# Performance work log

Measured on AMD Instinct MI355X. Metric: run time of the kernel, lower is better.

Reference implementation:

```python
import jax, jax.numpy as jnp
import numpy as np

NORM_EPS = 1e-6
QUANT_EPS = 1e-8


def setup_inputs() -> dict:
    key = jax.random.key(0)
    k1, k2 = jax.random.split(key)
    B, S, D_IN, D_OUT = 2, 4096, 2048, 2048
    x = jax.random.normal(k1, (B, S, D_IN), dtype=jnp.float32)
    # master fp32 weights (kaiming-uniform-ish scale)
    weight = jax.random.uniform(k2, (D_OUT, D_IN), dtype=jnp.float32,
                                minval=-1.0, maxval=1.0) * (1.0 / np.sqrt(D_IN))
    norm_weight = jnp.ones((D_IN,), dtype=jnp.float32)
    return {"x": x, "weight": weight, "norm_weight": norm_weight}


def _rmsnorm(x, gain):
    rms = jnp.sqrt(jnp.mean(x * x, axis=-1, keepdims=True) + NORM_EPS)
    return x / rms * gain


def _ternary_quantize(w):
    gamma = jnp.mean(jnp.abs(w))                       # absmean scale (scalar)
    w_q = jnp.clip(jnp.round(w / (gamma + QUANT_EPS)), -1.0, 1.0)
    return w_q, gamma


def reference(x, weight, norm_weight):
    # 1) RMSNorm input
    xn = _rmsnorm(x, norm_weight)
    # 2) ternary-quantize weights {-1,0,+1} with absmean gamma
    w_q, gamma = _ternary_quantize(weight)
    # 3) matmul with ternary weights, 4) scale by gamma
    # xn: [B,S,Din], w_q: [Dout,Din] -> [B,S,Dout]
    return jnp.einsum('bsd,od->bso', xn, w_q) * gamma
```

## Files before the change

### kernel.cpp

```cpp
#include <hip/hip_runtime.h>
#include <hip/hip_bf16.h>
#include <stdint.h>

typedef unsigned short u16;
typedef signed char i8;

#define D_INNER 2048
#define D_OUTER 2048
#define MROWS   8192
#define W_ELEMS (D_OUTER * D_INNER)
#define NPART   1024

#define BM 256
#define BN 256
#define BK 128
#define NKT (D_INNER / BK)
#define LDS_TOTAL 65536

typedef __attribute__((ext_vector_type(4))) float f32x4;
typedef __attribute__((ext_vector_type(4))) int   i32x4;
typedef __attribute__((ext_vector_type(16))) int  i32x16;

__global__ __launch_bounds__(256) void prep_kernel(const float* __restrict__ x,
                            const float* __restrict__ g,
                            const float* __restrict__ w,
                            i8* __restrict__ xn, float* __restrict__ srow,
                            float* __restrict__ partials) {
  __shared__ float red[4];
  __shared__ float redm[4];
  int t = threadIdx.x;
  int lane = t & 63, wvi = t >> 6;

  if (blockIdx.x >= MROWS) {
    int p = blockIdx.x - MROWS;
    int base = p * 1024;
    float s = 0.f;
#pragma unroll
    for (int r = 0; r < 4; ++r) {
      f32x4 v = ((const f32x4*)w)[base + r * 256 + t];
      s += fabsf(v[0]) + fabsf(v[1]) + fabsf(v[2]) + fabsf(v[3]);
    }
    for (int off = 32; off; off >>= 1) s += __shfl_down(s, off, 64);
    if (lane == 0) red[wvi] = s;
    __syncthreads();
    if (t == 0) partials[p] = red[0] + red[1] + red[2] + red[3];
    return;
  }

  int row = blockIdx.x;
  const f32x4* xr = (const f32x4*)(x + (size_t)row * D_INNER);
  i8* xo = xn + (size_t)row * D_INNER;

  f32x4 v0 = __builtin_nontemporal_load(&xr[t]);
  f32x4 v1 = __builtin_nontemporal_load(&xr[t + 256]);
  const f32x4* gr = (const f32x4*)g;
  f32x4 g0 = gr[t], g1 = gr[t + 256];

  float s = v0[0]*v0[0] + v0[1]*v0[1] + v0[2]*v0[2] + v0[3]*v0[3]
          + v1[0]*v1[0] + v1[1]*v1[1] + v1[2]*v1[2] + v1[3]*v1[3];
  float m = fmaxf(fmaxf(fmaxf(fabsf(v0[0]*g0[0]), fabsf(v0[1]*g0[1])),
                        fmaxf(fabsf(v0[2]*g0[2]), fabsf(v0[3]*g0[3]))),
                  fmaxf(fmaxf(fabsf(v1[0]*g1[0]), fabsf(v1[1]*g1[1])),
                        fmaxf(fabsf(v1[2]*g1[2]), fabsf(v1[3]*g1[3]))));
  for (int off = 32; off; off >>= 1) {
    s += __shfl_down(s, off, 64);
    m = fmaxf(m, __shfl_down(m, off, 64));
  }
  if (lane == 0) { red[wvi] = s; redm[wvi] = m; }
  __syncthreads();
  float total = red[0] + red[1] + red[2] + red[3];
  float rmax  = fmaxf(fmaxf(redm[0], redm[1]), fmaxf(redm[2], redm[3]));
  float invr = 1.0f / sqrtf(total * (1.0f / (float)D_INNER) + 1e-6f);

  float amax = fmaxf(rmax * invr, 1e-12f);
  float step = amax * (1.0f / 127.0f);
  float qs   = 127.0f / amax;
  if (t == 0) srow[row] = step;

  char4 q0, q1;
  float qv;
  qv = fminf(127.f, fmaxf(-127.f, rintf(v0[0]*invr*g0[0]*qs))); q0.x = (i8)(int)qv;
  qv = fminf(127.f, fmaxf(-127.f, rintf(v0[1]*invr*g0[1]*qs))); q0.y = (i8)(int)qv;
  qv = fminf(127.f, fmaxf(-127.f, rintf(v0[2]*invr*g0[2]*qs))); q0.z = (i8)(int)qv;
  qv = fminf(127.f, fmaxf(-127.f, rintf(v0[3]*invr*g0[3]*qs))); q0.w = (i8)(int)qv;
  qv = fminf(127.f, fmaxf(-127.f, rintf(v1[0]*invr*g1[0]*qs))); q1.x = (i8)(int)qv;
  qv = fminf(127.f, fmaxf(-127.f, rintf(v1[1]*invr*g1[1]*qs))); q1.y = (i8)(int)qv;
  qv = fminf(127.f, fmaxf(-127.f, rintf(v1[2]*invr*g1[2]*qs))); q1.z = (i8)(int)qv;
  qv = fminf(127.f, fmaxf(-127.f, rintf(v1[3]*invr*g1[3]*qs))); q1.w = (i8)(int)qv;
  ((char4*)xo)[t]       = q0;
  ((char4*)xo)[t + 256] = q1;
}

__global__ __launch_bounds__(256) void quant_kernel(const float* __restrict__ w,
                             const float* __restrict__ partials,
                             float* __restrict__ gamma_out, i8* __restrict__ wq) {
  f32x4 pv = ((const f32x4*)partials)[threadIdx.x];
  double d = (double)pv[0] + (double)pv[1] + (double)pv[2] + (double)pv[3];
  for (int off = 32; off; off >>= 1) d += __shfl_down(d, off, 64);
  __shared__ double red[4];
  int lane = threadIdx.x & 63, wvi = threadIdx.x >> 6;
  if (lane == 0) red[wvi] = d;
  __syncthreads();
  double total = red[0] + red[1] + red[2] + red[3];
  float gamma = (float)(total * (1.0 / (double)W_ELEMS));
  float inv = 1.0f / (gamma + 1e-8f);
  if (blockIdx.x == 0 && threadIdx.x == 0) *gamma_out = gamma;

  int tid = blockIdx.x * blockDim.x + threadIdx.x;
  int stride = gridDim.x * blockDim.x;
  for (int i = tid; i < W_ELEMS / 4; i += stride) {
    f32x4 v = ((const f32x4*)w)[i];
    char4 q;
    q.x = (i8)(int)fminf(1.f, fmaxf(-1.f, rintf(v[0] * inv)));
    q.y = (i8)(int)fminf(1.f, fmaxf(-1.f, rintf(v[1] * inv)));
    q.z = (i8)(int)fminf(1.f, fmaxf(-1.f, rintf(v[2] * inv)));
    q.w = (i8)(int)fminf(1.f, fmaxf(-1.f, rintf(v[3] * inv)));
    ((char4*)wq)[i] = q;
  }
}

#define GLDS(SRC, DST) __builtin_amdgcn_global_load_lds( \
    (const __attribute__((address_space(1))) void*)(SRC), \
    (__attribute__((address_space(3))) void*)(DST), 16, 0, 0)
#define WAITVM(N) asm volatile("s_waitcnt vmcnt(" #N ")")
#define BAR()     __builtin_amdgcn_s_barrier()
#define FENCE()   __builtin_amdgcn_sched_barrier(0)
#define LGKM0()   do { asm volatile("s_waitcnt lgkmcnt(0)"); FENCE(); } while (0)
#define BLOAD(DST, PTR, OFFS) \
  asm volatile("global_load_dwordx4 %0, %1, off offset:" OFFS \
               : "=v"(DST) : "v"(PTR))

__global__ __launch_bounds__(512, 2) void gemm_bt(const i8* __restrict__ A,
                                                  const i8* __restrict__ Bw,
                                                  const float* __restrict__ gamma_p,
                                                  const float* __restrict__ srow,
                                                  float* __restrict__ C) {
  extern __shared__ i8 lds[];

  int f   = blockIdx.y * 8 + blockIdx.x;
  int xcd = f & 7;
  int gg  = f >> 3;
  int nb  = (xcd & 1) * 4 + (gg & 3);
  int mb  = (xcd >> 1) * 8 + (gg >> 2);
  int bm0 = mb * BM;
  int bn0 = nb * BN;

  int tid  = threadIdx.x;
  int lane = tid & 63;
  int wv   = tid >> 6;
  int wr   = wv >> 2;
  int wc   = wv & 3;
  int l31  = lane & 31;
  int hi   = lane >> 5;

  const i8* Ag = A  + (size_t)bm0 * D_INNER;
  const i8* Bg = Bw + (size_t)bn0 * D_INNER;

  size_t a_src0 = (size_t)(tid >> 3) * D_INNER + (((tid & 7) ^ ((tid >> 3) & 7)) << 4);

  const i8* pB0 = Bg + (size_t)(wc * 64 +      l31) * D_INNER + hi * 16;
  const i8* pB1 = Bg + (size_t)(wc * 64 + 32 + l31) * D_INNER + hi * 16;

  int rdA = (wr * 128 + l31) * BK;
  int swz[4];
#pragma unroll
  for (int ks = 0; ks < 4; ++ks)
    swz[ks] = (((ks << 1) | hi) ^ (l31 & 7)) << 4;

  i32x16 acc[4][2] = {};
  i32x4 bfrA[4][2], bfrB[4][2];

#define STAGE_A(T_, S_) do { \
    _Pragma("unroll") for (int r = 0; r < 4; ++r) \
      GLDS(Ag + a_src0 + (size_t)r * (64 * D_INNER) + (size_t)(T_) * BK, \
           lds + (S_) * 32768 + r * 8192 + tid * 16); \
  } while (0)

#define BLOAD8(NXT) do { \
    BLOAD(NXT[0][0], pB0, "0");  BLOAD(NXT[0][1], pB1, "0");  \
    BLOAD(NXT[1][0], pB0, "32"); BLOAD(NXT[1][1], pB1, "32"); \
    BLOAD(NXT[2][0], pB0, "64"); BLOAD(NXT[2][1], pB1, "64"); \
    BLOAD(NXT[3][0], pB0, "96"); BLOAD(NXT[3][1], pB1, "96"); \
  } while (0)

#define MFMA8(PH, CUR) do { \
    __builtin_amdgcn_s_setprio(1); \
    _Pragma("unroll") for (int ks = 0; ks < 4; ++ks) { \
      acc[PH][0] = __builtin_amdgcn_mfma_i32_32x32x32_i8(af_[ks], CUR[ks][0], acc[PH][0], 0, 0, 0); \
      acc[PH][1] = __builtin_amdgcn_mfma_i32_32x32x32_i8(af_[ks], CUR[ks][1], acc[PH][1], 0, 0, 0); \
    } \
    __builtin_amdgcn_s_setprio(0); \
  } while (0)

#define TILE(T_, CUR, NXT, DO_STAGE, WAITSTMT) do { \
    if (DO_STAGE) { \
      BLOAD8(NXT); \
      STAGE_A((T_) + 1, ((T_) + 1) & 1); \
      pB0 += BK; pB1 += BK; \
    } \
    WAITSTMT; FENCE(); \
    BAR(); FENCE(); \
    { const i8* sl_ = lds + ((T_) & 1) * 32768; \
      _Pragma("unroll") for (int ph = 0; ph < 4; ++ph) { \
        i32x4 af_[4]; \
        _Pragma("unroll") for (int ks = 0; ks < 4; ++ks) \
          af_[ks] = *(const i32x4*)(sl_ + rdA + ph * 4096 + swz[ks]); \
        LGKM0(); \
        MFMA8(ph, CUR); \
      } } \
    BAR(); \
  } while (0)

  BLOAD8(bfrA);
  STAGE_A(0, 0);
  pB0 += BK; pB1 += BK;

  for (int t = 0; t < 14; t += 2) {
    TILE(t,     bfrA, bfrB, 1, WAITVM(12));
    TILE(t + 1, bfrB, bfrA, 1, WAITVM(12));
  }
  TILE(14, bfrA, bfrB, 1, WAITVM(12));
  TILE(15, bfrB, bfrA, 0, WAITVM(0));

  float gamma = *gamma_p;
  int colb = bn0 + wc * 64 + l31;
#pragma unroll
  for (int mi = 0; mi < 4; ++mi) {
    int rbase = bm0 + wr * 128 + mi * 32 + hi * 4;
    f32x4 sg[4];
#pragma unroll
    for (int q = 0; q < 4; ++q) {
      f32x4 sv = *(const f32x4*)(srow + rbase + q * 8);
      sg[q] = sv * gamma;
    }
#pragma unroll
    for (int nj = 0; nj < 2; ++nj) {
      i32x16 v = acc[mi][nj];
      float* cp = C + (size_t)rbase * D_OUTER + (colb + nj * 32);
#pragma unroll
      for (int q = 0; q < 4; ++q)
#pragma unroll
        for (int rr = 0; rr < 4; ++rr)
          cp[(size_t)(q * 8 + rr) * D_OUTER] = (float)v[q * 4 + rr] * sg[q][rr];
    }
  }
}

extern "C" void kernel_launch(void* const* d_in, const int* in_sizes, int n_in,
                              void* d_out, int out_size, void* d_ws, size_t ws_size,
                              hipStream_t stream) {
  const float* x = (const float*)d_in[0];
  const float* w = (const float*)d_in[1];
  const float* g = (const float*)d_in[2];
  float* out = (float*)d_out;

  float* gamma_p  = (float*)d_ws;
  float* partials = (float*)((char*)d_ws + 64);
  float* srow     = (float*)((char*)d_ws + 8192);
  i8* xn = (i8*)((char*)d_ws + 8192 + 32768);
  i8* wq = (i8*)((char*)d_ws + 8192 + 32768 + (size_t)MROWS * D_INNER);

  static bool attr_set = false;
  if (!attr_set) {
    (void)hipFuncSetAttribute(reinterpret_cast<const void*>(&gemm_bt),
                              hipFuncAttributeMaxDynamicSharedMemorySize, LDS_TOTAL);
    attr_set = true;
  }

  prep_kernel<<<MROWS + NPART, 256, 0, stream>>>(x, g, w, xn, srow, partials);
  quant_kernel<<<2048, 256, 0, stream>>>(w, partials, gamma_p, wq);
  gemm_bt<<<dim3(8, 32), 512, LDS_TOTAL, stream>>>(xn, wq, gamma_p, srow, out);
}
```

Before: 178.5 us.

## Stage B tiles through LDS, remap block tiles, and use wave-per-row prep

The GEMM now copies both the A and B tiles into LDS with global_load_lds, replacing the per-wave register loads of B. The LDS buffer doubles to 128KB for a two-slot double buffer. The block-to-tile mapping is changed to a simpler XCD-contiguous order. The RMSNorm/quant prep kernel now handles one row per wave using xor-shuffle reductions, which removes the LDS reduction and the block barrier. The larger LDS footprint likely drops occupancy from 2 blocks to 1 per CU, and the new tile mapping may change L2 reuse.

New measurement: 164.7 us. 7.7% less time.

```diff
diff --git a/kernel.cpp b/kernel.cpp
--- a/kernel.cpp
+++ b/kernel.cpp
@@ -15,7 +15,8 @@
 #define BN 256
 #define BK 128
 #define NKT (D_INNER / BK)
-#define LDS_TOTAL 65536
+#define SLOT_BYTES 65536
+#define LDS_TOTAL  131072
 
 typedef __attribute__((ext_vector_type(4))) float f32x4;
 typedef __attribute__((ext_vector_type(4))) int   i32x4;
@@ -26,13 +27,12 @@
                             const float* __restrict__ w,
                             i8* __restrict__ xn, float* __restrict__ srow,
                             float* __restrict__ partials) {
-  __shared__ float red[4];
-  __shared__ float redm[4];
   int t = threadIdx.x;
   int lane = t & 63, wvi = t >> 6;
 
-  if (blockIdx.x >= MROWS) {
-    int p = blockIdx.x - MROWS;
+  if (blockIdx.x >= MROWS / 4) {
+    __shared__ float red[4];
+    int p = blockIdx.x - MROWS / 4;
     int base = p * 1024;
     float s = 0.f;
 #pragma unroll
@@ -47,48 +47,45 @@
     return;
   }
 
-  int row = blockIdx.x;
+  int row = blockIdx.x * 4 + wvi;
   const f32x4* xr = (const f32x4*)(x + (size_t)row * D_INNER);
+  const f32x4* gr = (const f32x4*)g;
   i8* xo = xn + (size_t)row * D_INNER;
 
-  f32x4 v0 = __builtin_nontemporal_load(&xr[t]);
-  f32x4 v1 = __builtin_nontemporal_load(&xr[t + 256]);
-  const f32x4* gr = (const f32x4*)g;
-  f32x4 g0 = gr[t], g1 = gr[t + 256];
-
-  float s = v0[0]*v0[0] + v0[1]*v0[1] + v0[2]*v0[2] + v0[3]*v0[3]
-          + v1[0]*v1[0] + v1[1]*v1[1] + v1[2]*v1[2] + v1[3]*v1[3];
-  float m = fmaxf(fmaxf(fmaxf(fabsf(v0[0]*g0[0]), fabsf(v0[1]*g0[1])),
-                        fmaxf(fabsf(v0[2]*g0[2]), fabsf(v0[3]*g0[3]))),
-                  fmaxf(fmaxf(fabsf(v1[0]*g1[0]), fabsf(v1[1]*g1[1])),
-                        fmaxf(fabsf(v1[2]*g1[2]), fabsf(v1[3]*g1[3]))));
+  f32x4 v[8], gv[8];
+#pragma unroll
+  for (int r = 0; r < 8; ++r) {
+    v[r]  = __builtin_nontemporal_load(&xr[lane + r * 64]);
+    gv[r] = gr[lane + r * 64];
+  }
+  float s = 0.f, m = 0.f;
+#pragma unroll
+  for (int r = 0; r < 8; ++r) {
+    s += v[r][0]*v[r][0] + v[r][1]*v[r][1] + v[r][2]*v[r][2] + v[r][3]*v[r][3];
+    m = fmaxf(m, fmaxf(fmaxf(fabsf(v[r][0]*gv[r][0]), fabsf(v[r][1]*gv[r][1])),
+                       fmaxf(fabsf(v[r][2]*gv[r][2]), fabsf(v[r][3]*gv[r][3]))));
+  }
+#pragma unroll
   for (int off = 32; off; off >>= 1) {
-    s += __shfl_down(s, off, 64);
-    m = fmaxf(m, __shfl_down(m, off, 64));
-  }
-  if (lane == 0) { red[wvi] = s; redm[wvi] = m; }
-  __syncthreads();
-  float total = red[0] + red[1] + red[2] + red[3];
-  float rmax  = fmaxf(fmaxf(redm[0], redm[1]), fmaxf(redm[2], redm[3]));
-  float invr = 1.0f / sqrtf(total * (1.0f / (float)D_INNER) + 1e-6f);
-
-  float amax = fmaxf(rmax * invr, 1e-12f);
+    s += __shfl_xor(s, off, 64);
+    m = fmaxf(m, __shfl_xor(m, off, 64));
+  }
+  float invr = 1.0f / sqrtf(s * (1.0f / (float)D_INNER) + 1e-6f);
+  float amax = fmaxf(m * invr, 1e-12f);
   float step = amax * (1.0f / 127.0f);
   float qs   = 127.0f / amax;
-  if (t == 0) srow[row] = step;
-
-  char4 q0, q1;
-  float qv;
-  qv = fminf(127.f, fmaxf(-127.f, rintf(v0[0]*invr*g0[0]*qs))); q0.x = (i8)(int)qv;
-  qv = fminf(127.f, fmaxf(-127.f, rintf(v0[1]*invr*g0[1]*qs))); q0.y = (i8)(int)qv;
-  qv = fminf(127.f, fmaxf(-127.f, rintf(v0[2]*invr*g0[2]*qs))); q0.z = (i8)(int)qv;
-  qv = fminf(127.f, fmaxf(-127.f, rintf(v0[3]*invr*g0[3]*qs))); q0.w = (i8)(int)qv;
-  qv = fminf(127.f, fmaxf(-127.f, rintf(v1[0]*invr*g1[0]*qs))); q1.x = (i8)(int)qv;
-  qv = fminf(127.f, fmaxf(-127.f, rintf(v1[1]*invr*g1[1]*qs))); q1.y = (i8)(int)qv;
-  qv = fminf(127.f, fmaxf(-127.f, rintf(v1[2]*invr*g1[2]*qs))); q1.z = (i8)(int)qv;
-  qv = fminf(127.f, fmaxf(-127.f, rintf(v1[3]*invr*g1[3]*qs))); q1.w = (i8)(int)qv;
-  ((char4*)xo)[t]       = q0;
-  ((char4*)xo)[t + 256] = q1;
+  if (lane == 0) srow[row] = step;
+
+#pragma unroll
+  for (int r = 0; r < 8; ++r) {
+    char4 q;
+    float qv;
+    qv = fminf(127.f, fmaxf(-127.f, rintf(v[r][0]*invr*gv[r][0]*qs))); q.x = (i8)(int)qv;
+    qv = fminf(127.f, fmaxf(-127.f, rintf(v[r][1]*invr*gv[r][1]*qs))); q.y = (i8)(int)qv;
+    qv = fminf(127.f, fmaxf(-127.f, rintf(v[r][2]*invr*gv[r][2]*qs))); q.z = (i8)(int)qv;
+    qv = fminf(127.f, fmaxf(-127.f, rintf(v[r][3]*invr*gv[r][3]*qs))); q.w = (i8)(int)qv;
+    ((char4*)xo)[lane + r * 64] = q;
+  }
 }
 
 __global__ __launch_bounds__(256) void quant_kernel(const float* __restrict__ w,
@@ -125,10 +122,6 @@
 #define WAITVM(N) asm volatile("s_waitcnt vmcnt(" #N ")")
 #define BAR()     __builtin_amdgcn_s_barrier()
 #define FENCE()   __builtin_amdgcn_sched_barrier(0)
-#define LGKM0()   do { asm volatile("s_waitcnt lgkmcnt(0)"); FENCE(); } while (0)
-#define BLOAD(DST, PTR, OFFS) \
-  asm volatile("global_load_dwordx4 %0, %1, off offset:" OFFS \
-               : "=v"(DST) : "v"(PTR))
 
 __global__ __launch_bounds__(512, 2) void gemm_bt(const i8* __restrict__ A,
                                                   const i8* __restrict__ Bw,
@@ -140,8 +133,9 @@
   int f   = blockIdx.y * 8 + blockIdx.x;
   int xcd = f & 7;
   int gg  = f >> 3;
-  int nb  = (xcd & 1) * 4 + (gg & 3);
-  int mb  = (xcd >> 1) * 8 + (gg >> 2);
+  int orig = xcd * 32 + gg;
+  int nb  = orig & 7;
+  int mb  = orig >> 3;
   int bm0 = mb * BM;
   int bn0 = nb * BN;
 
@@ -156,71 +150,66 @@
   const i8* Ag = A  + (size_t)bm0 * D_INNER;
   const i8* Bg = Bw + (size_t)bn0 * D_INNER;
 
-  size_t a_src0 = (size_t)(tid >> 3) * D_INNER + (((tid & 7) ^ ((tid >> 3) & 7)) << 4);
-
-  const i8* pB0 = Bg + (size_t)(wc * 64 +      l31) * D_INNER + hi * 16;
-  const i8* pB1 = Bg + (size_t)(wc * 64 + 32 + l31) * D_INNER + hi * 16;
+  size_t src0 = (size_t)(tid >> 3) * D_INNER + (((tid & 7) ^ ((tid >> 3) & 7)) << 4);
+  int dst0 = tid * 16;
 
   int rdA = (wr * 128 + l31) * BK;
+  int rdB[2];
+  rdB[0] = 32768 + (wc * 64 +      l31) * BK;
+  rdB[1] = 32768 + (wc * 64 + 32 + l31) * BK;
   int swz[4];
 #pragma unroll
   for (int ks = 0; ks < 4; ++ks)
     swz[ks] = (((ks << 1) | hi) ^ (l31 & 7)) << 4;
 
   i32x16 acc[4][2] = {};
-  i32x4 bfrA[4][2], bfrB[4][2];
-
-#define STAGE_A(T_, S_) do { \
+
+#define STAGE_FULL(T_, S_) do { \
     _Pragma("unroll") for (int r = 0; r < 4; ++r) \
-      GLDS(Ag + a_src0 + (size_t)r * (64 * D_INNER) + (size_t)(T_) * BK, \
-           lds + (S_) * 32768 + r * 8192 + tid * 16); \
+      GLDS(Ag + src0 + (size_t)r * (64 * D_INNER) + (size_t)(T_) * BK, \
+           lds + (S_) * SLOT_BYTES + r * 8192 + dst0); \
+    _Pragma("unroll") for (int r = 0; r < 4; ++r) \
+      GLDS(Bg + src0 + (size_t)r * (64 * D_INNER) + (size_t)(T_) * BK, \
+           lds + (S_) * SLOT_BYTES + 32768 + r * 8192 + dst0); \
   } while (0)
 
-#define BLOAD8(NXT) do { \
-    BLOAD(NXT[0][0], pB0, "0");  BLOAD(NXT[0][1], pB1, "0");  \
-    BLOAD(NXT[1][0], pB0, "32"); BLOAD(NXT[1][1], pB1, "32"); \
-    BLOAD(NXT[2][0], pB0, "64"); BLOAD(NXT[2][1], pB1, "64"); \
-    BLOAD(NXT[3][0], pB0, "96"); BLOAD(NXT[3][1], pB1, "96"); \
+#define COMPUTE(T_) do { \
+    const i8* sl_ = lds + ((T_) & 1) * SLOT_BYTES; \
+    i32x4 bf_[4][2]; \
+    _Pragma("unroll") for (int ks = 0; ks < 4; ++ks) \
+      _Pragma("unroll") for (int nj = 0; nj < 2; ++nj) \
+        bf_[ks][nj] = *(const i32x4*)(sl_ + rdB[nj] + swz[ks]); \
+    _Pragma("unroll") for (int ph = 0; ph < 4; ++ph) { \
+      i32x4 af_[4]; \
+      _Pragma("unroll") for (int ks = 0; ks < 4; ++ks) \
+        af_[ks] = *(const i32x4*)(sl_ + rdA + ph * 4096 + swz[ks]); \
+      __builtin_amdgcn_s_setprio(1); \
+      _Pragma("unroll") for (int ks = 0; ks < 4; ++ks) { \
+        acc[ph][0] = __builtin_amdgcn_mfma_i32_32x32x32_i8(af_[ks], bf_[ks][0], acc[ph][0], 0, 0, 0); \
+        acc[ph][1] = __builtin_amdgcn_mfma_i32_32x32x32_i8(af_[ks], bf_[ks][1], acc[ph][1], 0, 0, 0); \
+      } \
+      __builtin_amdgcn_s_setprio(0); \
+    } \
   } while (0)
 
-#define MFMA8(PH, CUR) do { \
-    __builtin_amdgcn_s_setprio(1); \
-    _Pragma("unroll") for (int ks = 0; ks < 4; ++ks) { \
-      acc[PH][0] = __builtin_amdgcn_mfma_i32_32x32x32_i8(af_[ks], CUR[ks][0], acc[PH][0], 0, 0, 0); \
-      acc[PH][1] = __builtin_amdgcn_mfma_i32_32x32x32_i8(af_[ks], CUR[ks][1], acc[PH][1], 0, 0, 0); \
-    } \
-    __builtin_amdgcn_s_setprio(0); \
+#define TILE(T_, DO_STAGE, WAITSTMT) do { \
+    FENCE(); \
+    BAR();                        \
+    FENCE(); \
+    if (DO_STAGE) STAGE_FULL((T_) + 1, ((T_) + 1) & 1); \
+    FENCE(); \
+    WAITSTMT;                     \
+    FENCE(); \
+    BAR();                        \
+    FENCE(); \
+    COMPUTE(T_); \
   } while (0)
 
-#define TILE(T_, CUR, NXT, DO_STAGE, WAITSTMT) do { \
-    if (DO_STAGE) { \
-      BLOAD8(NXT); \
-      STAGE_A((T_) + 1, ((T_) + 1) & 1); \
-      pB0 += BK; pB1 += BK; \
-    } \
-    WAITSTMT; FENCE(); \
-    BAR(); FENCE(); \
-    { const i8* sl_ = lds + ((T_) & 1) * 32768; \
-      _Pragma("unroll") for (int ph = 0; ph < 4; ++ph) { \
-        i32x4 af_[4]; \
-        _Pragma("unroll") for (int ks = 0; ks < 4; ++ks) \
-          af_[ks] = *(const i32x4*)(sl_ + rdA + ph * 4096 + swz[ks]); \
-        LGKM0(); \
-        MFMA8(ph, CUR); \
-      } } \
-    BAR(); \
-  } while (0)
-
-  BLOAD8(bfrA);
-  STAGE_A(0, 0);
-  pB0 += BK; pB1 += BK;
-
-  for (int t = 0; t < 14; t += 2) {
-    TILE(t,     bfrA, bfrB, 1, WAITVM(12));
-    TILE(t + 1, bfrB, bfrA, 1, WAITVM(12));
-  }
-  TILE(14, bfrA, bfrB, 1, WAITVM(12));
-  TILE(15, bfrB, bfrA, 0, WAITVM(0));
+  STAGE_FULL(0, 0);
+
+  for (int t = 0; t < NKT - 1; ++t)
+    TILE(t, 1, WAITVM(8));
+  TILE(NKT - 1, 0, WAITVM(0));
 
   float gamma = *gamma_p;
   int colb = bn0 + wc * 64 + l31;
@@ -267,7 +256,7 @@
     attr_set = true;
   }
 
-  prep_kernel<<<MROWS + NPART, 256, 0, stream>>>(x, g, w, xn, srow, partials);
+  prep_kernel<<<MROWS / 4 + NPART, 256, 0, stream>>>(x, g, w, xn, srow, partials);
   quant_kernel<<<2048, 256, 0, stream>>>(w, partials, gamma_p, wq);
   gemm_bt<<<dim3(8, 32), 512, LDS_TOTAL, stream>>>(xn, wq, gamma_p, srow, out);
 }
```
